# Kernel tuning notes

Hardware: AMD Instinct MI355X
Metric: run time of the kernel (lower is better)

The kernel has to match this reference:

```python
import jax, jax.numpy as jnp
import numpy as np
import math

B, N, D = 128, 50, 256      # batch, segments per piece, cross-attn feature dim
H_CA = 8                    # cross-attention heads
FP, H_AP = 64, 8            # pooling feature dim / heads
S = N * N                   # flattened similarity length (<= 2560 pos-enc cap)
TEMP = 1.0
LN_EPS = 1e-5


def _ln(x, g, b):
    mu = jnp.mean(x, -1, keepdims=True)
    var = jnp.mean((x - mu) ** 2, -1, keepdims=True)
    return (x - mu) * jax.lax.rsqrt(var + LN_EPS) * g + b


def setup_inputs() -> dict:
    key = jax.random.key(0)
    ks = jax.random.split(key, 32)
    w = lambda i, shp, s=0.02: jax.random.normal(ks[i], shp, jnp.float32) * s
    z = lambda shp: jnp.zeros(shp, jnp.float32)
    o = lambda shp: jnp.ones(shp, jnp.float32)
    return {
        "features1": jax.random.normal(ks[0], (B, N, D), jnp.float32),
        "features2": jax.random.normal(ks[1], (B, N, D), jnp.float32),
        # CrossAttention (weights stored (in,out) so x @ W + b)
        "ca_wq": w(2, (D, D)), "ca_bq": z((D,)),
        "ca_wk": w(3, (D, D)), "ca_bk": z((D,)),
        "ca_wv": w(4, (D, D)), "ca_bv": z((D,)),
        "ca_wo": w(5, (D, D)), "ca_bo": z((D,)),
        "ca_ln1_g": o((D,)), "ca_ln1_b": z((D,)),
        "ca_ln2_g": o((D,)), "ca_ln2_b": z((D,)),
        "ca_w1": w(6, (D, 2 * D)), "ca_b1": z((2 * D,)),
        "ca_w2": w(7, (2 * D, D)), "ca_b2": z((D,)),
        # LearnableMetricSimilarity
        "ms_metric": jnp.eye(D, dtype=jnp.float32),
        "ms_wt": w(8, (D, D)), "ms_bt": z((D,)),
        # AttentionPooling
        "ap_wq": w(9, (1, FP)), "ap_bq": z((FP,)),
        "ap_wk": w(10, (1, FP)), "ap_bk": z((FP,)),
        "ap_wv": w(11, (1, FP)), "ap_bv": z((FP,)),
        "ap_pos": w(12, (1, 2560, FP), 0.02),
        "ap_wo": w(13, (FP, FP)), "ap_bo": z((FP,)),
        "ap_ln_g": o((FP,)), "ap_ln_b": z((FP,)),
    }


def reference(features1, features2,
              ca_wq, ca_bq, ca_wk, ca_bk, ca_wv, ca_bv, ca_wo, ca_bo,
              ca_ln1_g, ca_ln1_b, ca_ln2_g, ca_ln2_b,
              ca_w1, ca_b1, ca_w2, ca_b2,
              ms_metric, ms_wt, ms_bt,
              ap_wq, ap_bq, ap_wk, ap_bk, ap_wv, ap_bv,
              ap_pos, ap_wo, ap_bo, ap_ln_g, ap_ln_b):
    hd = D // H_CA

    def attend(fx, fy):
        q = (fx @ ca_wq + ca_bq).reshape(B, N, H_CA, hd)
        k = (fy @ ca_wk + ca_bk).reshape(B, N, H_CA, hd)
        v = (fy @ ca_wv + ca_bv).reshape(B, N, H_CA, hd)
        # Faithful to original: tensors stay (B,N,H,hd), so matmul with
        # k.transpose(-2,-1) yields per-position head-vs-head attention (B,N,H,H).
        scores = jnp.einsum('bnhd,bngd->bnhg', q, k) / math.sqrt(hd)
        wts = jax.nn.softmax(scores, axis=-1)  # dropout is identity (eval)
        att = jnp.einsum('bnhg,bngd->bnhd', wts, v).reshape(B, N, D)
        x = _ln(fx + att @ ca_wo + ca_bo, ca_ln1_g, ca_ln1_b)
        ffn = jax.nn.relu(x @ ca_w1 + ca_b1) @ ca_w2 + ca_b2
        return _ln(x + ffn, ca_ln2_g, ca_ln2_b)

    e1 = attend(features1, features2)
    e2 = attend(features2, features1)

    # Learnable metric similarity: Mahalanobis distance via quadratic expansion
    # d_ij = t1_i M t1_i + t2_j M t2_j - 2 t1_i M t2_j  (M symmetrized)
    t1 = e1 @ ms_wt + ms_bt
    t2 = e2 @ ms_wt + ms_bt
    M = (ms_metric + ms_metric.T) * 0.5
    t1M = t1 @ M
    t2M = t2 @ M
    q1 = jnp.sum(t1M * t1, axis=-1)                    # (B,N)
    q2 = jnp.sum(t2M * t2, axis=-1)                    # (B,N)
    cross = jnp.einsum('bnd,bmd->bnm', t1M, t2)        # (B,N,N)
    dist = q1[:, :, None] + q2[:, None, :] - 2.0 * cross
    sim = jnp.exp(jnp.clip(-dist / TEMP, -10.0, 10.0))  # (B,N,N)

    # Attention pooling over flattened similarity matrix
    flat = sim.reshape(B, S, 1)
    pos = ap_pos[:, :S, :]
    hdp = FP // H_AP
    q = (flat @ ap_wq + ap_bq + pos).reshape(B, S, H_AP, hdp)
    k = (flat @ ap_wk + ap_bk + pos).reshape(B, S, H_AP, hdp)
    v = (flat @ ap_wv + ap_bv).reshape(B, S, H_AP, hdp)
    scores = jnp.einsum('bshd,bsgd->bshg', q, k) / math.sqrt(hdp)  # (B,S,H,H)
    wts = jax.nn.softmax(scores, axis=-1)
    att = jnp.einsum('bshg,bsgd->bshd', wts, v).reshape(B, S, FP)
    pooled = jnp.mean(att, axis=1) @ ap_wo + ap_bo     # (B,FP)
    return _ln(pooled, ap_ln_g, ap_ln_b)
```

## Files before the change

kernel.cpp:

```cpp
#include <hip/hip_runtime.h>
#include <cstddef>
#include <cstdint>


namespace esn {

constexpr int kB   = 128;
constexpr int kN   = 50;
constexpr int kR   = kB * kN;
constexpr int kR2  = 2 * kR;
constexpr int kS   = kN * kN;

typedef __attribute__((ext_vector_type(8))) short short8;
typedef __attribute__((ext_vector_type(4))) float f32x4;

__device__ inline ushort f2bf_rn(float v) {
  uint32_t u = __float_as_uint(v);
  uint32_t r = (u + 0x7fffu + ((u >> 16) & 1u)) >> 16;
  return (ushort)r;
}
__device__ inline float bf2f(ushort b) {
  return __uint_as_float(((uint32_t)b) << 16);
}
__device__ inline void split2(float v, ushort& h, ushort& l) {
  h = f2bf_rn(v);
  l = f2bf_rn(v - bf2f(h));
}

__device__ __forceinline__ void gld16(const ushort* g, ushort* l) {
  __builtin_amdgcn_global_load_lds(
      (const __attribute__((address_space(1))) void*)g,
      (__attribute__((address_space(3))) void*)l,
      16, 0, 0);
}

template<bool RELU, bool WF32, bool WSPLIT>
__global__ __launch_bounds__(256)
void gemm_mfma_kernel(const ushort* __restrict__ Ah, const ushort* __restrict__ Al, int lda,
                      const ushort* __restrict__ Bh, const ushort* __restrict__ Bl, int ldb,
                      const float* __restrict__ bias,
                      float* __restrict__ C, int ldc,
                      ushort* __restrict__ Ch, ushort* __restrict__ Cl,
                      int K)
{
  __shared__ __align__(16) ushort sAh[128 * 32];
  __shared__ __align__(16) ushort sAl[128 * 32];
  __shared__ __align__(16) ushort sBh[128 * 32];
  __shared__ __align__(16) ushort sBl[128 * 32];

  const int tid  = threadIdx.x;
  const int lane = tid & 63;
  const int wave = tid >> 6;
  const int wm   = wave >> 1, wn = wave & 1;
  const int bm   = blockIdx.x * 128, bn = blockIdx.y * 128;

  const int lrow  = lane >> 2;
  const int lslot = lane & 3;

  f32x4 acc[4][4] = {};

  const int nK = K >> 5;
  for (int kt = 0; kt < nK; kt++) {
    const int kk = kt << 5;
#pragma unroll
    for (int i = 0; i < 2; i++) {
      const int grp  = wave * 32 + i * 16;
      const int row  = grp + lrow;
      const int c    = lslot ^ ((row >> 1) & 3);
      const size_t aoff = (size_t)(bm + row) * lda + kk + c * 8;
      const size_t boff = (size_t)(bn + row) * ldb + kk + c * 8;
      gld16(Ah + aoff, sAh + grp * 32);
      gld16(Al + aoff, sAl + grp * 32);
      gld16(Bh + boff, sBh + grp * 32);
      gld16(Bl + boff, sBl + grp * 32);
    }
    __syncthreads();

    const int r16 = lane & 15, kq = lane >> 4;
    short8 afh[4], afl[4], bfh[4], bfl[4];
#pragma unroll
    for (int f = 0; f < 4; f++) {
      int arow = wm * 64 + f * 16 + r16;
      int sa = kq ^ ((arow >> 1) & 3);
      afh[f] = *(const short8*)(sAh + arow * 32 + sa * 8);
      afl[f] = *(const short8*)(sAl + arow * 32 + sa * 8);
      int brow = wn * 64 + f * 16 + r16;
      int sb = kq ^ ((brow >> 1) & 3);
      bfh[f] = *(const short8*)(sBh + brow * 32 + sb * 8);
      bfl[f] = *(const short8*)(sBl + brow * 32 + sb * 8);
    }
#pragma unroll
    for (int mf = 0; mf < 4; mf++)
#pragma unroll
      for (int nf = 0; nf < 4; nf++) {
        acc[mf][nf] = __builtin_amdgcn_mfma_f32_16x16x32_bf16(afh[mf], bfh[nf], acc[mf][nf], 0, 0, 0);
        acc[mf][nf] = __builtin_amdgcn_mfma_f32_16x16x32_bf16(afh[mf], bfl[nf], acc[mf][nf], 0, 0, 0);
        acc[mf][nf] = __builtin_amdgcn_mfma_f32_16x16x32_bf16(afl[mf], bfh[nf], acc[mf][nf], 0, 0, 0);
      }
    __syncthreads();
  }

  const int r16 = lane & 15, rq = lane >> 4;
#pragma unroll
  for (int nf = 0; nf < 4; nf++) {
    int col = bn + wn * 64 + nf * 16 + r16;
    float bv = bias ? bias[col] : 0.0f;
#pragma unroll
    for (int mf = 0; mf < 4; mf++) {
      int rowb = bm + wm * 64 + mf * 16 + rq * 4;
#pragma unroll
      for (int r = 0; r < 4; r++) {
        float v = acc[mf][nf][r] + bv;
        if (RELU) v = fmaxf(v, 0.0f);
        size_t off = (size_t)(rowb + r) * ldc + col;
        if (WF32) C[off] = v;
        if (WSPLIT) {
          ushort h, l; split2(v, h, l);
          Ch[off] = h; Cl[off] = l;
        }
      }
    }
  }
}

__global__ void prep_w_kernel(const float* __restrict__ wq, const float* __restrict__ wk,
                              const float* __restrict__ wv, const float* __restrict__ bq,
                              const float* __restrict__ bk, const float* __restrict__ bv,
                              const float* __restrict__ wo, const float* __restrict__ w1,
                              const float* __restrict__ w2, const float* __restrict__ wt,
                              const float* __restrict__ msm,
                              ushort* __restrict__ qkvh, ushort* __restrict__ qkvl,
                              ushort* __restrict__ woh,  ushort* __restrict__ wol,
                              ushort* __restrict__ w1h,  ushort* __restrict__ w1l,
                              ushort* __restrict__ w2h,  ushort* __restrict__ w2l,
                              ushort* __restrict__ wth,  ushort* __restrict__ wtl,
                              ushort* __restrict__ msh,  ushort* __restrict__ msl,
                              float* __restrict__ bqkv)
{
  int idx = blockIdx.x * 256 + threadIdx.x;
  if (idx < 768)
    bqkv[idx] = idx < 256 ? bq[idx] : idx < 512 ? bk[idx - 256] : bv[idx - 512];
  float v; ushort *oh, *ol; int off;
  if (idx < 196608) {
    int n = idx >> 8, k = idx & 255;
    v = n < 256 ? wq[k * 256 + n] : n < 512 ? wk[k * 256 + n - 256] : wv[k * 256 + n - 512];
    oh = qkvh; ol = qkvl; off = idx;
  } else if (idx < 262144) {
    int i = idx - 196608; int n = i >> 8, k = i & 255;
    v = wo[k * 256 + n]; oh = woh; ol = wol; off = i;
  } else if (idx < 393216) {
    int i = idx - 262144; int n = i >> 8, k = i & 255;
    v = w1[k * 512 + n]; oh = w1h; ol = w1l; off = i;
  } else if (idx < 524288) {
    int i = idx - 393216; int n = i >> 9, k = i & 511;
    v = w2[k * 256 + n]; oh = w2h; ol = w2l; off = i;
  } else if (idx < 589824) {
    int i = idx - 524288; int n = i >> 8, k = i & 255;
    v = wt[k * 256 + n]; oh = wth; ol = wtl; off = i;
  } else if (idx < 655360) {
    int i = idx - 589824; int n = i >> 8, k = i & 255;
    v = 0.5f * (msm[k * 256 + n] + msm[n * 256 + k]); oh = msh; ol = msl; off = i;
  } else return;
  ushort h, l; split2(v, h, l);
  oh[off] = h; ol[off] = l;
}

__global__ void split_f_kernel(const float* __restrict__ f1, const float* __restrict__ f2,
                               ushort* __restrict__ Fh, ushort* __restrict__ Fl)
{
  int idx = (blockIdx.x * 256 + threadIdx.x) * 4;
  const float* src = idx < kR * 256 ? f1 + idx : f2 + (idx - kR * 256);
  float4 v = *(const float4*)src;
  ushort h, l;
  split2(v.x, h, l); Fh[idx + 0] = h; Fl[idx + 0] = l;
  split2(v.y, h, l); Fh[idx + 1] = h; Fl[idx + 1] = l;
  split2(v.z, h, l); Fh[idx + 2] = h; Fl[idx + 2] = l;
  split2(v.w, h, l); Fh[idx + 3] = h; Fl[idx + 3] = l;
}

__global__ __launch_bounds__(256)
void ca_attn_kernel(const float* __restrict__ P, ushort* __restrict__ Ah,
                    ushort* __restrict__ Al)
{
  const int rib  = threadIdx.x >> 6;
  const int row  = blockIdx.x * 4 + rib;
  const int lane = threadIdx.x & 63;
  const int partner = (row < kR) ? row + kR : row - kR;
  const float* q = P + (size_t)row * 768;
  const float* k = P + (size_t)partner * 768 + 256;
  const float* v = P + (size_t)partner * 768 + 512;
  const int h = lane >> 3, g = lane & 7;

  float s = 0.0f;
#pragma unroll
  for (int i = 0; i < 8; i++) {
    float4 qa = *(const float4*)(q + h * 32 + i * 4);
    float4 ka = *(const float4*)(k + g * 32 + i * 4);
    s = fmaf(qa.x, ka.x, s); s = fmaf(qa.y, ka.y, s);
    s = fmaf(qa.z, ka.z, s); s = fmaf(qa.w, ka.w, s);
  }
  s *= 0.17677669529663687f;

  float mx = s;
#pragma unroll
  for (int d = 1; d < 8; d <<= 1) mx = fmaxf(mx, __shfl_xor(mx, d));
  float e = expf(s - mx);
  float se = e;
#pragma unroll
  for (int d = 1; d < 8; d <<= 1) se += __shfl_xor(se, d);
  float w = e / se;

  __shared__ float lds_w[4][64];
  lds_w[rib][lane] = w;
  __syncthreads();

  const int dc = lane & 7;
  float o[4] = {};
#pragma unroll
  for (int gg = 0; gg < 8; gg++) {
    float wg = lds_w[rib][h * 8 + gg];
    float4 va = *(const float4*)(v + gg * 32 + dc * 4);
    o[0] = fmaf(wg, va.x, o[0]); o[1] = fmaf(wg, va.y, o[1]);
    o[2] = fmaf(wg, va.z, o[2]); o[3] = fmaf(wg, va.w, o[3]);
  }
  size_t base = (size_t)row * 256 + h * 32 + dc * 4;
#pragma unroll
  for (int j = 0; j < 4; j++) {
    ushort hh, ll; split2(o[j], hh, ll);
    Ah[base + j] = hh; Al[base + j] = ll;
  }
}

template<bool WF32>
__global__ __launch_bounds__(256)
void ln_res_kernel(const float* __restrict__ Y, const float* __restrict__ R1,
                   const float* __restrict__ R2, const float* __restrict__ g,
                   const float* __restrict__ b, float* __restrict__ X,
                   ushort* __restrict__ Xh, ushort* __restrict__ Xl)
{
  const int row  = blockIdx.x * 4 + (threadIdx.x >> 6);
  const int lane = threadIdx.x & 63;
  const float* res = (row < kR) ? (R1 + (size_t)row * 256)
                                : (R2 + (size_t)(row - kR) * 256);
  float4 y4 = *(const float4*)(Y + (size_t)row * 256 + lane * 4);
  float4 r4 = *(const float4*)(res + lane * 4);
  float v[4] = {y4.x + r4.x, y4.y + r4.y, y4.z + r4.z, y4.w + r4.w};

  float ssum = v[0] + v[1] + v[2] + v[3];
#pragma unroll
  for (int d = 1; d < 64; d <<= 1) ssum += __shfl_xor(ssum, d);
  float mu = ssum * (1.0f / 256.0f);
  float qq = 0.0f;
#pragma unroll
  for (int j = 0; j < 4; j++) { float dv = v[j] - mu; qq = fmaf(dv, dv, qq); }
#pragma unroll
  for (int d = 1; d < 64; d <<= 1) qq += __shfl_xor(qq, d);
  float rstd = rsqrtf(qq * (1.0f / 256.0f) + 1e-5f);

  float4 g4 = *(const float4*)(g + lane * 4);
  float4 b4 = *(const float4*)(b + lane * 4);
  float o[4];
  o[0] = (v[0] - mu) * rstd * g4.x + b4.x;
  o[1] = (v[1] - mu) * rstd * g4.y + b4.y;
  o[2] = (v[2] - mu) * rstd * g4.z + b4.z;
  o[3] = (v[3] - mu) * rstd * g4.w + b4.w;
  size_t base = (size_t)row * 256 + lane * 4;
  if (WF32) *(float4*)(X + base) = *(float4*)o;
#pragma unroll
  for (int j = 0; j < 4; j++) {
    ushort hh, ll; split2(o[j], hh, ll);
    Xh[base + j] = hh; Xl[base + j] = ll;
  }
}

__global__ __launch_bounds__(256)
void qdot_kernel(const float* __restrict__ T, const float* __restrict__ TM,
                 float* __restrict__ QD)
{
  const int row  = blockIdx.x * 4 + (threadIdx.x >> 6);
  const int lane = threadIdx.x & 63;
  float4 a = *(const float4*)(T  + (size_t)row * 256 + lane * 4);
  float4 b = *(const float4*)(TM + (size_t)row * 256 + lane * 4);
  float s = a.x * b.x + a.y * b.y + a.z * b.z + a.w * b.w;
#pragma unroll
  for (int d = 1; d < 64; d <<= 1) s += __shfl_xor(s, d);
  if (lane == 0) QD[row] = s;
}

__global__ __launch_bounds__(256)
void cross_kernel(const float* __restrict__ T1M, const float* __restrict__ T2,
                  float* __restrict__ CP)
{
  const int b  = blockIdx.x >> 1;
  const int kh = blockIdx.x & 1;
  __shared__ float sA[128][64];
  __shared__ float sB[128][64];
  const int tid = threadIdx.x;
#pragma unroll
  for (int i = 0; i < 8; i++) {
    int slot = tid + i * 256;
    int n  = slot >> 5;
    int k4 = (slot & 31) * 4;
    float4 a = make_float4(0.f, 0.f, 0.f, 0.f), c = a;
    if (n < 50) {
      a = *(const float4*)(T1M + ((size_t)b * 50 + n) * 256 + kh * 128 + k4);
      c = *(const float4*)(T2  + ((size_t)kR + b * 50 + n) * 256 + kh * 128 + k4);
    }
    sA[k4 + 0][n] = a.x; sA[k4 + 1][n] = a.y; sA[k4 + 2][n] = a.z; sA[k4 + 3][n] = a.w;
    sB[k4 + 0][n] = c.x; sB[k4 + 1][n] = c.y; sB[k4 + 2][n] = c.z; sB[k4 + 3][n] = c.w;
  }
  __syncthreads();
  const int tn = tid & 15, tm = tid >> 4;
  const int n0 = tn * 4, m0 = tm * 4;
  float acc[4][4] = {};
  for (int k = 0; k < 128; k++) {
    float4 a4 = *(const float4*)(&sA[k][n0]);
    float4 b4 = *(const float4*)(&sB[k][m0]);
    float a[4] = {a4.x, a4.y, a4.z, a4.w};
    float c[4] = {b4.x, b4.y, b4.z, b4.w};
#pragma unroll
    for (int i = 0; i < 4; i++)
#pragma unroll
      for (int j = 0; j < 4; j++)
        acc[i][j] = fmaf(a[i], c[j], acc[i][j]);
  }
#pragma unroll
  for (int i = 0; i < 4; i++) {
    float* cp = CP + (((size_t)b * 2 + kh) * 64 + n0 + i) * 64 + m0;
    *(float4*)cp = *(float4*)(&acc[i][0]);
  }
}

__global__ void sim_kernel(const float* __restrict__ CP, const float* __restrict__ QD,
                           float* __restrict__ SIM)
{
  int idx = blockIdx.x * 256 + threadIdx.x;
  if (idx >= kB * kS) return;
  int b = idx / kS, s = idx % kS;
  int n = s / kN, m = s % kN;
  float c = CP[(((size_t)b * 2 + 0) * 64 + n) * 64 + m]
          + CP[(((size_t)b * 2 + 1) * 64 + n) * 64 + m];
  float dist = QD[b * kN + n] + QD[kR + b * kN + m] - 2.0f * c;
  float z = -dist;
  z = fminf(fmaxf(z, -10.0f), 10.0f);
  SIM[idx] = expf(z);
}

__global__ __launch_bounds__(256)
void ap_tables_kernel(const float* __restrict__ pos,
                      const float* __restrict__ wq, const float* __restrict__ bq,
                      const float* __restrict__ wk, const float* __restrict__ bk,
                      float2* __restrict__ TT)
{
  int idx = blockIdx.x * 256 + threadIdx.x;
  if (idx >= kS * 64) return;
  int s = idx >> 6, lane = idx & 63;
  int h = lane >> 3, g = lane & 7;
  float t1 = 0.f, t0 = 0.f;
#pragma unroll
  for (int d = 0; d < 8; d++) {
    float a  = wq[h * 8 + d];
    float c  = bq[h * 8 + d] + pos[s * 64 + h * 8 + d];
    float bb = wk[g * 8 + d];
    float e  = bk[g * 8 + d] + pos[s * 64 + g * 8 + d];
    t1 = fmaf(a, e, t1);
    t1 = fmaf(c, bb, t1);
    t0 = fmaf(c, e, t0);
  }
  TT[idx] = make_float2(t1, t0);
}

__global__ __launch_bounds__(256)
void ap_kernel(const float* __restrict__ SIM, const float2* __restrict__ TT,
               const float* __restrict__ wq, const float* __restrict__ wk,
               float* __restrict__ GP)
{
  const int b    = blockIdx.x;
  const int sb   = blockIdx.y;
  const int wave = threadIdx.x >> 6, lane = threadIdx.x & 63;
  const int strip = sb * 4 + wave;
  const int h = lane >> 3, g = lane & 7;

  float A2 = 0.f;
#pragma unroll
  for (int d = 0; d < 8; d++) A2 = fmaf(wq[h * 8 + d], wk[g * 8 + d], A2);
  const float inv8 = 0.35355339059327373f;

  float G0 = 0.f, G1 = 0.f;
  const int s0 = strip * 79;
  const int s1 = (s0 + 79 < kS) ? s0 + 79 : kS;
  for (int s = s0; s < s1; s++) {
    float f = SIM[(size_t)b * kS + s];
    float2 t = TT[s * 64 + lane];
    float x = fmaf(f * f, A2, fmaf(f, t.x, t.y)) * inv8;
    float mx = x;
    mx = fmaxf(mx, __shfl_xor(mx, 1));
    mx = fmaxf(mx, __shfl_xor(mx, 2));
    mx = fmaxf(mx, __shfl_xor(mx, 4));
    float e = __expf(x - mx);
    float se = e;
    se += __shfl_xor(se, 1);
    se += __shfl_xor(se, 2);
    se += __shfl_xor(se, 4);
    float w = e / se;
    G0 += w;
    G1 = fmaf(w, f, G1);
  }
  float* gp = GP + (((size_t)b * 32 + strip) * 2) * 64;
  gp[lane]      = G1;
  gp[64 + lane] = G0;
}

__global__ __launch_bounds__(64)
void final_kernel(const float* __restrict__ GP, const float* __restrict__ wv,
                  const float* __restrict__ bv, const float* __restrict__ wo,
                  const float* __restrict__ bo, const float* __restrict__ lg,
                  const float* __restrict__ lb, float* __restrict__ out)
{
  const int b = blockIdx.x, j = threadIdx.x;
  float G1 = 0.f, G0 = 0.f;
  for (int st = 0; st < 32; st++) {
    const float* gp = GP + (((size_t)b * 32 + st) * 2) * 64;
    G1 += gp[j];
    G0 += gp[64 + j];
  }
  __shared__ float sg1[64], sg0[64];
  sg1[j] = G1; sg0[j] = G0;
  __syncthreads();
  const int h = j >> 3, d = j & 7;
  float acc = 0.f;
#pragma unroll
  for (int g = 0; g < 8; g++) {
    acc = fmaf(sg1[h * 8 + g], wv[g * 8 + d], acc);
    acc = fmaf(sg0[h * 8 + g], bv[g * 8 + d], acc);
  }
  double pooled = (double)acc / 2500.0;
  __shared__ double sp[64];
  sp[j] = pooled;
  __syncthreads();
  double o = (double)bo[j];
  for (int dd = 0; dd < 64; dd++) o += sp[dd] * (double)wo[dd * 64 + j];
  double ssum = o;
#pragma unroll
  for (int d2 = 1; d2 < 64; d2 <<= 1) ssum += __shfl_xor(ssum, d2);
  double mu = ssum / 64.0;
  double dv = o - mu;
  double qq = dv * dv;
#pragma unroll
  for (int d2 = 1; d2 < 64; d2 <<= 1) qq += __shfl_xor(qq, d2);
  double var = qq / 64.0;
  double r = 1.0 / sqrt(var + 1e-5);
  out[(size_t)b * 64 + j] = (float)(dv * r * (double)lg[j] + (double)lb[j]);
}

}

extern "C" void kernel_launch(void* const* d_in, const int* in_sizes, int n_in,
                              void* d_out, int out_size, void* d_ws, size_t ws_size,
                              hipStream_t stream)
{
  using namespace esn;
  const float* f1      = (const float*)d_in[0];
  const float* f2      = (const float*)d_in[1];
  const float* ca_wq   = (const float*)d_in[2];
  const float* ca_bq   = (const float*)d_in[3];
  const float* ca_wk   = (const float*)d_in[4];
  const float* ca_bk   = (const float*)d_in[5];
  const float* ca_wv   = (const float*)d_in[6];
  const float* ca_bv   = (const float*)d_in[7];
  const float* ca_wo   = (const float*)d_in[8];
  const float* ca_bo   = (const float*)d_in[9];
  const float* ln1_g   = (const float*)d_in[10];
  const float* ln1_b   = (const float*)d_in[11];
  const float* ln2_g   = (const float*)d_in[12];
  const float* ln2_b   = (const float*)d_in[13];
  const float* ca_w1   = (const float*)d_in[14];
  const float* ca_b1   = (const float*)d_in[15];
  const float* ca_w2   = (const float*)d_in[16];
  const float* ca_b2   = (const float*)d_in[17];
  const float* ms_met  = (const float*)d_in[18];
  const float* ms_wt   = (const float*)d_in[19];
  const float* ms_bt   = (const float*)d_in[20];
  const float* ap_wq   = (const float*)d_in[21];
  const float* ap_bq   = (const float*)d_in[22];
  const float* ap_wk   = (const float*)d_in[23];
  const float* ap_bk   = (const float*)d_in[24];
  const float* ap_wv   = (const float*)d_in[25];
  const float* ap_bv   = (const float*)d_in[26];
  const float* ap_pos  = (const float*)d_in[27];
  const float* ap_wo   = (const float*)d_in[28];
  const float* ap_bo   = (const float*)d_in[29];
  const float* ap_ln_g = (const float*)d_in[30];
  const float* ap_ln_b = (const float*)d_in[31];

  float* ws = (float*)d_ws;
  float*  P    = ws;
  ushort* Hh   = (ushort*)(ws);
  ushort* Hl   = (ushort*)(ws + 3276800);
  float*  TM   = ws;
  ushort* Th   = (ushort*)(ws + 3276800);
  ushort* Tl   = (ushort*)(ws + 4915200);
  float*  Tt   = ws + 6553600;
  ushort* S1h  = (ushort*)(ws + 9830400);
  ushort* S1l  = (ushort*)(ws + 11468800);
  float*  X    = ws + 13107200;
  float*  Y    = ws + 16384000;
  float*  CP   = ws + 16384000;
  float*  SIM  = ws + 17432576;
  float*  GP   = ws + 17752576;
  float2* TT   = (float2*)(ws + 18399744);
  float*  QD   = ws + 19660800;
  ushort* Wqh  = (ushort*)(ws + 19673600);
  ushort* Wql  = (ushort*)(ws + 19771904);
  ushort* Woh  = (ushort*)(ws + 19870208);
  ushort* Wol  = (ushort*)(ws + 19902976);
  ushort* W1h  = (ushort*)(ws + 19935744);
  ushort* W1l  = (ushort*)(ws + 20001280);
  ushort* W2h  = (ushort*)(ws + 20066816);
  ushort* W2l  = (ushort*)(ws + 20132352);
  ushort* Wth  = (ushort*)(ws + 20197888);
  ushort* Wtl  = (ushort*)(ws + 20230656);
  ushort* Msh  = (ushort*)(ws + 20263424);
  ushort* Msl  = (ushort*)(ws + 20296192);
  float*  BQKV = ws + 20328960;

  prep_w_kernel<<<2560, 256, 0, stream>>>(ca_wq, ca_wk, ca_wv, ca_bq, ca_bk, ca_bv,
                                          ca_wo, ca_w1, ca_w2, ms_wt, ms_met,
                                          Wqh, Wql, Woh, Wol, W1h, W1l, W2h, W2l,
                                          Wth, Wtl, Msh, Msl, BQKV);
  split_f_kernel<<<3200, 256, 0, stream>>>(f1, f2, S1h, S1l);
  ap_tables_kernel<<<625, 256, 0, stream>>>(ap_pos, ap_wq, ap_bq, ap_wk, ap_bk, TT);
  gemm_mfma_kernel<false, true, false><<<dim3(100, 6), 256, 0, stream>>>(
      S1h, S1l, 256, Wqh, Wql, 256, BQKV, P, 768, nullptr, nullptr, 256);
  ca_attn_kernel<<<kR2 / 4, 256, 0, stream>>>(P, S1h, S1l);
  gemm_mfma_kernel<false, true, false><<<dim3(100, 2), 256, 0, stream>>>(
      S1h, S1l, 256, Woh, Wol, 256, ca_bo, Y, 256, nullptr, nullptr, 256);
  ln_res_kernel<true><<<kR2 / 4, 256, 0, stream>>>(Y, f1, f2, ln1_g, ln1_b, X, S1h, S1l);
  gemm_mfma_kernel<true, false, true><<<dim3(100, 4), 256, 0, stream>>>(
      S1h, S1l, 256, W1h, W1l, 256, ca_b1, nullptr, 512, Hh, Hl, 256);
  gemm_mfma_kernel<false, true, false><<<dim3(100, 2), 256, 0, stream>>>(
      Hh, Hl, 512, W2h, W2l, 512, ca_b2, Y, 256, nullptr, nullptr, 512);
  ln_res_kernel<false><<<kR2 / 4, 256, 0, stream>>>(Y, X, X + (size_t)kR * 256,
                                                    ln2_g, ln2_b, nullptr, S1h, S1l);
  gemm_mfma_kernel<false, true, true><<<dim3(100, 2), 256, 0, stream>>>(
      S1h, S1l, 256, Wth, Wtl, 256, ms_bt, Tt, 256, Th, Tl, 256);
  gemm_mfma_kernel<false, true, false><<<dim3(100, 2), 256, 0, stream>>>(
      Th, Tl, 256, Msh, Msl, 256, nullptr, TM, 256, nullptr, nullptr, 256);
  qdot_kernel<<<kR2 / 4, 256, 0, stream>>>(Tt, TM, QD);
  cross_kernel<<<kB * 2, 256, 0, stream>>>(TM, Tt, CP);
  sim_kernel<<<(kB * kS + 255) / 256, 256, 0, stream>>>(CP, QD, SIM);
  ap_kernel<<<dim3(kB, 8), 256, 0, stream>>>(SIM, TT, ap_wq, ap_wk, GP);
  final_kernel<<<kB, 64, 0, stream>>>(GP, ap_wv, ap_bv, ap_wo, ap_bo,
                                      ap_ln_g, ap_ln_b, (float*)d_out);
}
```

Measured before the change: 253.5 us.

## Double-buffer GEMM LDS tiles and restructure attention-pooling softmax per lane

The MFMA GEMM now double-buffers its LDS tiles, issuing the next K-slice global-to-LDS loads before computing on the current one and dropping one barrier per iteration. This is meant to hide global load latency behind MFMA work, at the cost of doubled shared memory, which may lower occupancy. The attention-pooling kernel is also reorganized. Each lane now owns one head and computes all 8 softmax logits itself, with 8 sequence positions handled in parallel per wave. This replaces the per-position shuffle reductions with in-register max and sum, followed by a shuffle reduction across positions at the end.

```diff
diff --git a/kernel.cpp b/kernel.cpp
--- a/kernel.cpp
+++ b/kernel.cpp
@@ -43,10 +43,10 @@
                       ushort* __restrict__ Ch, ushort* __restrict__ Cl,
                       int K)
 {
-  __shared__ __align__(16) ushort sAh[128 * 32];
-  __shared__ __align__(16) ushort sAl[128 * 32];
-  __shared__ __align__(16) ushort sBh[128 * 32];
-  __shared__ __align__(16) ushort sBl[128 * 32];
+  __shared__ __align__(16) ushort sAh[2][128 * 32];
+  __shared__ __align__(16) ushort sAl[2][128 * 32];
+  __shared__ __align__(16) ushort sBh[2][128 * 32];
+  __shared__ __align__(16) ushort sBl[2][128 * 32];
 
   const int tid  = threadIdx.x;
   const int lane = tid & 63;
@@ -59,8 +59,7 @@
 
   f32x4 acc[4][4] = {};
 
-  const int nK = K >> 5;
-  for (int kt = 0; kt < nK; kt++) {
+  auto stage = [&](int buf, int kt) {
     const int kk = kt << 5;
 #pragma unroll
     for (int i = 0; i < 2; i++) {
@@ -69,12 +68,19 @@
       const int c    = lslot ^ ((row >> 1) & 3);
       const size_t aoff = (size_t)(bm + row) * lda + kk + c * 8;
       const size_t boff = (size_t)(bn + row) * ldb + kk + c * 8;
-      gld16(Ah + aoff, sAh + grp * 32);
-      gld16(Al + aoff, sAl + grp * 32);
-      gld16(Bh + boff, sBh + grp * 32);
-      gld16(Bl + boff, sBl + grp * 32);
-    }
+      gld16(Ah + aoff, &sAh[buf][grp * 32]);
+      gld16(Al + aoff, &sAl[buf][grp * 32]);
+      gld16(Bh + boff, &sBh[buf][grp * 32]);
+      gld16(Bl + boff, &sBl[buf][grp * 32]);
+    }
+  };
+
+  const int nK = K >> 5;
+  stage(0, 0);
+  int cur = 0;
+  for (int kt = 0; kt < nK; kt++) {
     __syncthreads();
+    if (kt + 1 < nK) stage(cur ^ 1, kt + 1);
 
     const int r16 = lane & 15, kq = lane >> 4;
     short8 afh[4], afl[4], bfh[4], bfl[4];
@@ -82,12 +88,12 @@
     for (int f = 0; f < 4; f++) {
       int arow = wm * 64 + f * 16 + r16;
       int sa = kq ^ ((arow >> 1) & 3);
-      afh[f] = *(const short8*)(sAh + arow * 32 + sa * 8);
-      afl[f] = *(const short8*)(sAl + arow * 32 + sa * 8);
+      afh[f] = *(const short8*)(&sAh[cur][arow * 32 + sa * 8]);
+      afl[f] = *(const short8*)(&sAl[cur][arow * 32 + sa * 8]);
       int brow = wn * 64 + f * 16 + r16;
       int sb = kq ^ ((brow >> 1) & 3);
-      bfh[f] = *(const short8*)(sBh + brow * 32 + sb * 8);
-      bfl[f] = *(const short8*)(sBl + brow * 32 + sb * 8);
+      bfh[f] = *(const short8*)(&sBh[cur][brow * 32 + sb * 8]);
+      bfl[f] = *(const short8*)(&sBl[cur][brow * 32 + sb * 8]);
     }
 #pragma unroll
     for (int mf = 0; mf < 4; mf++)
@@ -97,7 +103,7 @@
         acc[mf][nf] = __builtin_amdgcn_mfma_f32_16x16x32_bf16(afh[mf], bfl[nf], acc[mf][nf], 0, 0, 0);
         acc[mf][nf] = __builtin_amdgcn_mfma_f32_16x16x32_bf16(afl[mf], bfh[nf], acc[mf][nf], 0, 0, 0);
       }
-    __syncthreads();
+    cur ^= 1;
   }
 
   const int r16 = lane & 15, rq = lane >> 4;
@@ -379,36 +385,71 @@
   const int sb   = blockIdx.y;
   const int wave = threadIdx.x >> 6, lane = threadIdx.x & 63;
   const int strip = sb * 4 + wave;
-  const int h = lane >> 3, g = lane & 7;
-
-  float A2 = 0.f;
-#pragma unroll
-  for (int d = 0; d < 8; d++) A2 = fmaf(wq[h * 8 + d], wk[g * 8 + d], A2);
+  const int sIdx = lane >> 3;
+  const int h    = lane & 7;
+
+  float wqr[8];
+#pragma unroll
+  for (int d = 0; d < 8; d++) wqr[d] = wq[h * 8 + d];
+  float A2[8];
+#pragma unroll
+  for (int g = 0; g < 8; g++) {
+    float a = 0.f;
+#pragma unroll
+    for (int d = 0; d < 8; d++) a = fmaf(wqr[d], wk[g * 8 + d], a);
+    A2[g] = a;
+  }
   const float inv8 = 0.35355339059327373f;
 
-  float G0 = 0.f, G1 = 0.f;
+  float G0[8] = {}, G1[8] = {};
   const int s0 = strip * 79;
-  const int s1 = (s0 + 79 < kS) ? s0 + 79 : kS;
-  for (int s = s0; s < s1; s++) {
-    float f = SIM[(size_t)b * kS + s];
-    float2 t = TT[s * 64 + lane];
-    float x = fmaf(f * f, A2, fmaf(f, t.x, t.y)) * inv8;
-    float mx = x;
-    mx = fmaxf(mx, __shfl_xor(mx, 1));
-    mx = fmaxf(mx, __shfl_xor(mx, 2));
-    mx = fmaxf(mx, __shfl_xor(mx, 4));
-    float e = __expf(x - mx);
-    float se = e;
-    se += __shfl_xor(se, 1);
-    se += __shfl_xor(se, 2);
-    se += __shfl_xor(se, 4);
-    float w = e / se;
-    G0 += w;
-    G1 = fmaf(w, f, G1);
-  }
-  float* gp = GP + (((size_t)b * 32 + strip) * 2) * 64;
-  gp[lane]      = G1;
-  gp[64 + lane] = G0;
+  for (int it = 0; it < 10; it++) {
+    int rel = it * 8 + sIdx;
+    int s   = s0 + rel;
+    bool valid = (rel < 79) && (s < kS);
+    int sc = valid ? s : (kS - 1);
+    float f = SIM[(size_t)b * kS + sc];
+    const float4* tp = (const float4*)(TT + sc * 64 + h * 8);
+    float4 t01 = tp[0], t23 = tp[1], t45 = tp[2], t67 = tp[3];
+    float f2 = f * f;
+    float x[8];
+    x[0] = fmaf(f2, A2[0], fmaf(f, t01.x, t01.y)) * inv8;
+    x[1] = fmaf(f2, A2[1], fmaf(f, t01.z, t01.w)) * inv8;
+    x[2] = fmaf(f2, A2[2], fmaf(f, t23.x, t23.y)) * inv8;
+    x[3] = fmaf(f2, A2[3], fmaf(f, t23.z, t23.w)) * inv8;
+    x[4] = fmaf(f2, A2[4], fmaf(f, t45.x, t45.y)) * inv8;
+    x[5] = fmaf(f2, A2[5], fmaf(f, t45.z, t45.w)) * inv8;
+    x[6] = fmaf(f2, A2[6], fmaf(f, t67.x, t67.y)) * inv8;
+    x[7] = fmaf(f2, A2[7], fmaf(f, t67.z, t67.w)) * inv8;
+    float mx = fmaxf(fmaxf(fmaxf(x[0], x[1]), fmaxf(x[2], x[3])),
+                     fmaxf(fmaxf(x[4], x[5]), fmaxf(x[6], x[7])));
+    float e[8], se = 0.f;
+#pragma unroll
+    for (int g = 0; g < 8; g++) { e[g] = __expf(x[g] - mx); se += e[g]; }
+    float inv = valid ? (1.0f / se) : 0.0f;
+#pragma unroll
+    for (int g = 0; g < 8; g++) {
+      float w = e[g] * inv;
+      G0[g] += w;
+      G1[g] = fmaf(w, f, G1[g]);
+    }
+  }
+#pragma unroll
+  for (int m = 8; m <= 32; m <<= 1) {
+#pragma unroll
+    for (int g = 0; g < 8; g++) {
+      G0[g] += __shfl_xor(G0[g], m);
+      G1[g] += __shfl_xor(G1[g], m);
+    }
+  }
+  if (sIdx == 0) {
+    float* gp = GP + (((size_t)b * 32 + strip) * 2) * 64;
+#pragma unroll
+    for (int g = 0; g < 8; g++) {
+      gp[h * 8 + g]      = G1[g];
+      gp[64 + h * 8 + g] = G0[g];
+    }
+  }
 }
 
 __global__ __launch_bounds__(64)
```

Measured after the change: 213.1 us. -16.0%, faster.
